# Performance work log

Hardware: AMD Instinct MI355X
Metric: run time of the kernel (lower is better)

Reference implementation:

```python
import jax, jax.numpy as jnp
import numpy as np

B, S, IN, EMB, H = 4, 2048, 256, 512, 8
D = EMB // H
SCALE = 1.0 / np.sqrt(EMB)  # source uses 1/sqrt(embed_size), not head_dim
EPS = 1e-5


def setup_inputs() -> dict:
    key = jax.random.key(0)
    ks = jax.random.split(key, 20)
    def w(k, shape, fan_in):
        return jax.random.normal(k, shape, jnp.float32) * (1.0 / np.sqrt(fan_in))
    inp = {"state_emb": jax.random.normal(ks[0], (B, S, IN), jnp.float32)}
    i = 1
    for p in ("q", "k", "v"):
        inp[f"{p}_W1"] = w(ks[i], (IN, EMB), IN); i += 1
        inp[f"{p}_b1"] = jnp.zeros((EMB,), jnp.float32)
        inp[f"{p}_W2"] = w(ks[i], (EMB, EMB), EMB); i += 1
        inp[f"{p}_b2"] = jnp.zeros((EMB,), jnp.float32)
    inp["f_W1"] = w(ks[i], (EMB, 2 * EMB), EMB); i += 1
    inp["f_b1"] = jnp.zeros((2 * EMB,), jnp.float32)
    inp["f_W2"] = w(ks[i], (2 * EMB, EMB), 2 * EMB); i += 1
    inp["f_b2"] = jnp.zeros((EMB,), jnp.float32)
    inp["ln1_g"] = jnp.ones((EMB,), jnp.float32)
    inp["ln1_b"] = jnp.zeros((EMB,), jnp.float32)
    inp["ln2_g"] = jnp.ones((EMB,), jnp.float32)
    inp["ln2_b"] = jnp.zeros((EMB,), jnp.float32)
    return inp


def _mlp2(x, W1, b1, W2, b2):
    return jax.nn.relu(x @ W1 + b1) @ W2 + b2


def _layernorm(x, g, b):
    mu = jnp.mean(x, axis=-1, keepdims=True)
    var = jnp.mean(jnp.square(x - mu), axis=-1, keepdims=True)
    return (x - mu) * jax.lax.rsqrt(var + EPS) * g + b


def reference(state_emb, q_W1, q_b1, q_W2, q_b2, k_W1, k_b1, k_W2, k_b2,
              v_W1, v_b1, v_W2, v_b2, f_W1, f_b1, f_W2, f_b2,
              ln1_g, ln1_b, ln2_g, ln2_b):
    n, dim = state_emb.shape[0], state_emb.shape[1]
    q = _mlp2(state_emb, q_W1, q_b1, q_W2, q_b2)  # [n, dim, EMB]
    k = _mlp2(state_emb, k_W1, k_b1, k_W2, k_b2)
    v = _mlp2(state_emb, v_W1, v_b1, v_W2, v_b2)
    qh = q.reshape(n, dim, H, D)
    kh = k.reshape(n, dim, H, D)
    vh = v.reshape(n, dim, H, D)
    energy = jnp.einsum('nqhd,nkhd->nhqk', qh, kh)  # [n, H, dim, dim]
    attn = jax.nn.softmax(energy * SCALE, axis=-1)
    ctx = jnp.einsum('nhql,nlhd->nqhd', attn, vh).reshape(n, dim, EMB)
    x = _layernorm(ctx + q, ln1_g, ln1_b)  # residual with queries, per source
    ff = _mlp2(x, f_W1, f_b1, f_W2, f_b2)
    return _layernorm(x + ff, ln2_g, ln2_b)
```

## Files before the change

### kernel.cpp

```cpp
#include <hip/hip_runtime.h>
#include <hip/hip_bf16.h>
#include <math.h>

#define BB   4
#define SS   2048
#define INF_ 256
#define EMB  512
#define NH   8
#define HD   64
#define NT   8192

typedef unsigned short u16;
typedef unsigned int   u32;
typedef __attribute__((ext_vector_type(8))) short bf16x8;
typedef __attribute__((ext_vector_type(8))) unsigned short u16x8;
typedef __attribute__((ext_vector_type(4))) float f32x4;

constexpr float C2  = 0.06375871607f;
constexpr float TB  = 1.00390625f;
constexpr float EPS = 1e-5f;

__device__ __forceinline__ u16 f2bf(float v) {
    __hip_bfloat16 h = __float2bfloat16(v);
    return *(u16*)&h;
}
__device__ __forceinline__ float bf2f(u16 u) {
    __hip_bfloat16 h = *(__hip_bfloat16*)&u;
    return __bfloat162float(h);
}
__device__ __forceinline__ u16 ftrunc_bf(float v) {
    return (u16)(__float_as_uint(v * TB) >> 16);
}
__device__ __forceinline__ f32x4 mfma16(bf16x8 a, bf16x8 b, f32x4 c) {
    return __builtin_amdgcn_mfma_f32_16x16x32_bf16(a, b, c, 0, 0, 0);
}
__device__ __forceinline__ void async16(const void* g, void* l) {
    __builtin_amdgcn_global_load_lds(
        (const __attribute__((address_space(1))) void*)g,
        (__attribute__((address_space(3))) void*)l, 16, 0, 0);
}
__device__ __forceinline__ int derive_flag(const u16* x) {
    const int lane = threadIdx.x & 63;
    const unsigned e = (x[lane * 2] >> 7) & 0xFF;
    float pl = (e == 0 || (e >= 110 && e <= 140)) ? 1.0f : 0.0f;
    #pragma unroll
    for (int o = 1; o < 64; o <<= 1) pl += __shfl_xor(pl, o);
    return pl < 32.0f;
}

__global__ __launch_bounds__(256) void prep(
    const u16* __restrict__ xsrc,
    const void* w0, const void* w1, const void* w2, const void* w3,
    const void* w4, const void* w5, const void* w6, const void* w7,
    const void* p0, const void* p1, const void* p2, const void* p3,
    const void* p4, const void* p5, const void* p6, const void* p7,
    const void* p8, const void* p9, const void* p10, const void* p11,
    u16* __restrict__ xbf, u16* __restrict__ wt1, u16* __restrict__ wt2,
    u16* __restrict__ f1t, u16* __restrict__ f2t, float* __restrict__ small)
{
    const int isf = derive_flag(xsrc);
    const int z = blockIdx.z;
    const int tid = threadIdx.x;

    if (z < 8) {
        int K, M; const void* src; u16* dst;
        switch (z) {
            case 0: K=256;  M=512;  src=w0; dst=wt1;             break;
            case 1: K=256;  M=512;  src=w1; dst=wt1+512*256;     break;
            case 2: K=256;  M=512;  src=w2; dst=wt1+2*512*256;   break;
            case 3: K=512;  M=512;  src=w3; dst=wt2;             break;
            case 4: K=512;  M=512;  src=w4; dst=wt2+512*512;     break;
            case 5: K=512;  M=512;  src=w5; dst=wt2+2*512*512;   break;
            case 6: K=512;  M=1024; src=w6; dst=f1t;             break;
            default:K=1024; M=512;  src=w7; dst=f2t;             break;
        }
        const int m0 = blockIdx.x * 32, k0 = blockIdx.y * 32;
        if (m0 >= M || k0 >= K) return;
        __shared__ u16 t[32][33];
        const int tx = tid & 31, ty = tid >> 5;
        #pragma unroll
        for (int i = 0; i < 4; ++i) {
            const int kk = k0 + ty + i * 8;
            t[ty + i * 8][tx] = isf ? ftrunc_bf(((const float*)src)[(size_t)kk * M + m0 + tx])
                                    : ((const u16*)src)[(size_t)kk * M + m0 + tx];
        }
        __syncthreads();
        #pragma unroll
        for (int i = 0; i < 4; ++i) {
            const int mm = m0 + ty + i * 8;
            dst[(size_t)mm * K + k0 + tx] = t[tx][ty + i * 8];
        }
    } else if (z == 8) {
        const int bid = blockIdx.y * 32 + blockIdx.x;
        const int base = bid * 2048 + tid * 8;
        if (isf) {
            #pragma unroll
            for (int j = 0; j < 8; ++j)
                xbf[base + j] = ftrunc_bf(((const float*)xsrc)[base + j]);
        } else {
            *(u16x8*)&xbf[base] = *(const u16x8*)&xsrc[base];
        }
    } else {
        const int bid = blockIdx.y * 32 + blockIdx.x;
        if (bid >= 28) return;
        const int e = bid * 256 + tid;
        int id, i;
        if (e < 3072)      { id = e >> 9;               i = e & 511;          }
        else if (e < 4096) { id = 6;                    i = e - 3072;         }
        else               { id = 7 + ((e - 4096) >> 9); i = (e - 4096) & 511; }
        const void* src;
        switch (id) {
            case 0: src = p0; break;  case 1: src = p1; break;
            case 2: src = p2; break;  case 3: src = p3; break;
            case 4: src = p4; break;  case 5: src = p5; break;
            case 6: src = p6; break;  case 7: src = p7; break;
            case 8: src = p8; break;  case 9: src = p9; break;
            case 10: src = p10; break; default: src = p11; break;
        }
        small[e] = isf ? ((const float*)src)[i] : bf2f(((const u16*)src)[i]);
    }
}

template <bool RELU, bool AWHICH, bool VOUT, bool SCALEK>
__global__ __launch_bounds__(256) void gemm64(
    const u16* __restrict__ Aall, const u16* __restrict__ Wtall,
    const float* __restrict__ ball, u16* __restrict__ out,
    u16* __restrict__ vtb, int N, int K, int M)
{
    __shared__ __align__(16) u16 sA[64 * 64];
    __shared__ __align__(16) u16 sB[64 * 64];

    const int mtiles = M >> 6;
    const int which = blockIdx.y / mtiles;
    const int colb  = blockIdx.y % mtiles;
    const int row0 = blockIdx.x << 6, col0 = colb << 6;
    const u16* A  = Aall + (AWHICH ? (size_t)which * N * K : 0);
    const u16* Wt = Wtall + (size_t)which * M * K;
    const float* bias = ball + (size_t)which * M;

    const int tid = threadIdx.x;
    const int lane = tid & 63, w = tid >> 6;
    const int wrow = (w & 1) << 5, wcol = (w >> 1) << 5;
    const int c = lane & 15, quad = lane >> 4;

    const u16* ap[2]; const u16* bp[2];
    #pragma unroll
    for (int i = 0; i < 2; ++i) {
        const int raw = i * 256 + tid, r = raw >> 3, ch = (raw & 7) ^ (r & 7);
        ap[i] = A + (size_t)(row0 + r) * K + ch * 8;
        bp[i] = Wt + (size_t)(col0 + r) * K + ch * 8;
    }

    f32x4 acc[2][2] = {};

    for (int k0 = 0; k0 < K; k0 += 64) {
        __syncthreads();
        #pragma unroll
        for (int i = 0; i < 2; ++i) {
            async16(ap[i], (char*)sA + (i * 256 + tid) * 16);
            ap[i] += 64;
            async16(bp[i], (char*)sB + (i * 256 + tid) * 16);
            bp[i] += 64;
        }
        __syncthreads();

        #pragma unroll
        for (int kt = 0; kt < 2; ++kt) {
            bf16x8 af[2], bfr[2];
            #pragma unroll
            for (int rt = 0; rt < 2; ++rt) {
                const int r = wrow + rt * 16 + c;
                af[rt] = *(const bf16x8*)&sA[(r * 8 + ((kt * 4 + quad) ^ (r & 7))) * 8];
            }
            #pragma unroll
            for (int ct = 0; ct < 2; ++ct) {
                const int r = wcol + ct * 16 + c;
                bfr[ct] = *(const bf16x8*)&sB[(r * 8 + ((kt * 4 + quad) ^ (r & 7))) * 8];
            }
            #pragma unroll
            for (int rt = 0; rt < 2; ++rt)
                #pragma unroll
                for (int ct = 0; ct < 2; ++ct)
                    acc[rt][ct] = mfma16(af[rt], bfr[ct], acc[rt][ct]);
        }
    }

    if (VOUT && which == 2) {
        __syncthreads();
        #pragma unroll
        for (int rt = 0; rt < 2; ++rt) {
            const int rowb = wrow + rt * 16 + quad * 4;
            #pragma unroll
            for (int ct = 0; ct < 2; ++ct) {
                const int col = wcol + ct * 16 + c;
                const float bb = bias[col0 + col];
                ushort4 pk;
                pk.x = ftrunc_bf(acc[rt][ct][0] + bb);
                pk.y = ftrunc_bf(acc[rt][ct][1] + bb);
                pk.z = ftrunc_bf(acc[rt][ct][2] + bb);
                pk.w = ftrunc_bf(acc[rt][ct][3] + bb);
                *(ushort4*)&sA[col * 72 + rowb] = pk;
            }
        }
        __syncthreads();
        const int dl = tid >> 2, part = tid & 3;
        const int hg = (col0 + dl) >> 6, dd = (col0 + dl) & 63;
        const int bb = row0 >> 11, s0 = row0 & 2047;
        u16* dst = vtb + ((size_t)(bb * NH + hg) * HD + dd) * SS + s0 + part * 16;
        #pragma unroll
        for (int j = 0; j < 2; ++j)
            *(u16x8*)&dst[j * 8] = *(const u16x8*)&sA[dl * 72 + part * 16 + j * 8];
        return;
    }

    const float sc = (SCALEK && which == 1) ? C2 : 1.0f;
    const size_t outW = (size_t)which * N * M;
    #pragma unroll
    for (int rt = 0; rt < 2; ++rt) {
        #pragma unroll
        for (int i = 0; i < 4; ++i) {
            const int row = row0 + wrow + rt * 16 + quad * 4 + i;
            #pragma unroll
            for (int ct = 0; ct < 2; ++ct) {
                const int col = col0 + wcol + ct * 16 + c;
                float v = (acc[rt][ct][i] + bias[col]) * sc;
                if (RELU) v = fmaxf(v, 0.0f);
                out[outW + (size_t)row * M + col] = ftrunc_bf(v);
            }
        }
    }
}

__global__ __launch_bounds__(512) void attn_mfma(
    const u16* __restrict__ q, const u16* __restrict__ k,
    const u16* __restrict__ vt, u16* __restrict__ ctx)
{
    __shared__ __align__(16) u16 sK[2][64 * 64];
    __shared__ __align__(16) u16 sV[2][64 * 64];
    __shared__ __align__(16) u16 sP[16][16 * 64];

    const int tid = threadIdx.x;
    const int w = tid >> 6, lane = tid & 63;
    const int c = lane & 15, quad = lane >> 4;
    const int id = blockIdx.x;
    const int slot = id >> 3;
    const int bh = ((id & 7) << 2) | (slot >> 3);
    const int qt = slot & 7;
    const int b = bh >> 3, h = bh & 7;
    const int q0 = qt * 256;
    const size_t tokbase = (size_t)b * SS;
    const int hoff = h * HD;

    bf16x8 qf[2][2];
    #pragma unroll
    for (int f = 0; f < 2; ++f) {
        const int myq = q0 + w * 32 + f * 16 + c;
        #pragma unroll
        for (int kt = 0; kt < 2; ++kt)
            qf[f][kt] = *(const bf16x8*)&q[(tokbase + myq) * EMB + hoff + kt * 32 + quad * 8];
    }

    union { u32 u[4]; bf16x8 v; } ones;
    #pragma unroll
    for (int i = 0; i < 4; ++i) ones.u[i] = 0x3F803F80u;

    const u16* kp; const u16* vp;
    {
        const int rr = tid >> 3, ch = (tid & 7) ^ (rr & 7);
        kp = k + (tokbase + rr) * EMB + hoff + ch * 8;
        vp = vt + ((size_t)(b * NH + h) * HD + rr) * SS + ch * 8;
    }
    auto stage = [&](int buf) {
        async16(kp, (char*)&sK[buf][0] + tid * 16);
        kp += 64 * EMB;
        async16(vp, (char*)&sV[buf][0] + tid * 16);
        vp += 64;
    };
    stage(0);

    f32x4 accO[2][4] = {};
    f32x4 accL[2] = {};
    const f32x4 zc = {};

    for (int t = 0; t < SS / 64; ++t) {
        __syncthreads();
        const int buf = t & 1;
        if (t + 1 < SS / 64) stage(buf ^ 1);

        f32x4 accS[2][4];
        #pragma unroll
        for (int mt = 0; mt < 4; ++mt) {
            const int key = mt * 16 + c;
            bf16x8 kf0 = *(const bf16x8*)&sK[buf][(key * 8 + (quad ^ (key & 7))) * 8];
            #pragma unroll
            for (int f = 0; f < 2; ++f)
                accS[f][mt] = mfma16(kf0, qf[f][0], zc);
            bf16x8 kf1 = *(const bf16x8*)&sK[buf][(key * 8 + ((4 + quad) ^ (key & 7))) * 8];
            #pragma unroll
            for (int f = 0; f < 2; ++f)
                accS[f][mt] = mfma16(kf1, qf[f][1], accS[f][mt]);
        }

        #pragma unroll
        for (int f = 0; f < 2; ++f) {
            u32 pw[8];
            #pragma unroll
            for (int mt = 0; mt < 4; ++mt) {
                const float e0 = __builtin_amdgcn_exp2f(accS[f][mt][0]);
                const float e1 = __builtin_amdgcn_exp2f(accS[f][mt][1]);
                const float e2 = __builtin_amdgcn_exp2f(accS[f][mt][2]);
                const float e3 = __builtin_amdgcn_exp2f(accS[f][mt][3]);
                pw[2 * mt]     = __builtin_amdgcn_perm(__float_as_uint(e1), __float_as_uint(e0), 0x07060302u);
                pw[2 * mt + 1] = __builtin_amdgcn_perm(__float_as_uint(e3), __float_as_uint(e2), 0x07060302u);
            }
            #pragma unroll
            for (int mt = 0; mt < 4; ++mt) {
                const int chunkW = 2 * mt + (quad >> 1);
                const int blk = c * 8 + (chunkW ^ (c & 7));
                uint2 u; u.x = pw[2 * mt]; u.y = pw[2 * mt + 1];
                *(uint2*)((char*)&sP[w * 2 + f][0] + blk * 16 + 8 * (quad & 1)) = u;
            }
        }

        bf16x8 pf[2][2];
        #pragma unroll
        for (int f = 0; f < 2; ++f) {
            #pragma unroll
            for (int kt = 0; kt < 2; ++kt)
                pf[f][kt] = *(const bf16x8*)&sP[w * 2 + f][(c * 8 + ((kt * 4 + quad) ^ (c & 7))) * 8];
            accL[f] = mfma16(ones.v, pf[f][0], accL[f]);
            accL[f] = mfma16(ones.v, pf[f][1], accL[f]);
        }
        #pragma unroll
        for (int nt = 0; nt < 4; ++nt) {
            const int d = nt * 16 + c;
            #pragma unroll
            for (int kt = 0; kt < 2; ++kt) {
                bf16x8 vf = *(const bf16x8*)&sV[buf][(d * 8 + ((kt * 4 + quad) ^ (d & 7))) * 8];
                #pragma unroll
                for (int f = 0; f < 2; ++f)
                    accO[f][nt] = mfma16(vf, pf[f][kt], accO[f][nt]);
            }
        }
    }

    #pragma unroll
    for (int f = 0; f < 2; ++f) {
        const float l = accL[f][0];
        const float li = (l > 0.0f) ? (1.0f / l) : 0.0f;
        const int tok = q0 + w * 32 + f * 16 + c;
        u16* dst = ctx + (tokbase + tok) * EMB + hoff + quad * 4;
        #pragma unroll
        for (int nt = 0; nt < 4; ++nt) {
            ushort4 pk;
            pk.x = ftrunc_bf(accO[f][nt][0] * li);
            pk.y = ftrunc_bf(accO[f][nt][1] * li);
            pk.z = ftrunc_bf(accO[f][nt][2] * li);
            pk.w = ftrunc_bf(accO[f][nt][3] * li);
            *(ushort4*)&dst[nt * 16] = pk;
        }
    }
}

__global__ __launch_bounds__(256) void ln_mid(
    const u16* __restrict__ a, const u16* __restrict__ b2,
    const float* __restrict__ g, const float* __restrict__ be,
    u16* __restrict__ outb)
{
    const int wave = threadIdx.x >> 6, lane = threadIdx.x & 63;
    const size_t row = (size_t)blockIdx.x * 4 + wave;
    const u16x8 av = *(const u16x8*)&a[row * EMB + lane * 8];
    const u16x8 bv = *(const u16x8*)&b2[row * EMB + lane * 8];
    float vals[8], sum = 0.0f;
    #pragma unroll
    for (int i = 0; i < 8; ++i) { vals[i] = bf2f(av[i]) + bf2f(bv[i]); sum += vals[i]; }
    #pragma unroll
    for (int o = 1; o < 64; o <<= 1) sum += __shfl_xor(sum, o);
    const float mu = sum * (1.0f / 512.0f);
    float vs = 0.0f;
    #pragma unroll
    for (int i = 0; i < 8; ++i) { const float d = vals[i] - mu; vs += d * d; }
    #pragma unroll
    for (int o = 1; o < 64; o <<= 1) vs += __shfl_xor(vs, o);
    const float rstd = rsqrtf(vs * (1.0f / 512.0f) + EPS);
    u16x8 ov;
    #pragma unroll
    for (int i = 0; i < 8; ++i) {
        const int col = lane * 8 + i;
        ov[i] = f2bf((vals[i] - mu) * rstd * g[col] + be[col]);
    }
    *(u16x8*)&outb[row * EMB + lane * 8] = ov;
}

__global__ __launch_bounds__(256) void ln_final(
    const u16* __restrict__ a, const u16* __restrict__ b2,
    const float* __restrict__ g, const float* __restrict__ be,
    void* __restrict__ dout, const u16* __restrict__ xsrc)
{
    const int isf = derive_flag(xsrc);
    const int wave = threadIdx.x >> 6, lane = threadIdx.x & 63;
    const size_t row = (size_t)blockIdx.x * 4 + wave;
    const u16x8 av = *(const u16x8*)&a[row * EMB + lane * 8];
    const u16x8 bv = *(const u16x8*)&b2[row * EMB + lane * 8];
    float vals[8], sum = 0.0f;
    #pragma unroll
    for (int i = 0; i < 8; ++i) { vals[i] = bf2f(av[i]) + bf2f(bv[i]); sum += vals[i]; }
    #pragma unroll
    for (int o = 1; o < 64; o <<= 1) sum += __shfl_xor(sum, o);
    const float mu = sum * (1.0f / 512.0f);
    float vs = 0.0f;
    #pragma unroll
    for (int i = 0; i < 8; ++i) { const float d = vals[i] - mu; vs += d * d; }
    #pragma unroll
    for (int o = 1; o < 64; o <<= 1) vs += __shfl_xor(vs, o);
    const float rstd = rsqrtf(vs * (1.0f / 512.0f) + EPS);
    if (isf) {
        #pragma unroll
        for (int i = 0; i < 8; ++i) {
            const int col = lane * 8 + i;
            ((float*)dout)[row * EMB + col] = (vals[i] - mu) * rstd * g[col] + be[col];
        }
    } else {
        u16x8 ov;
        #pragma unroll
        for (int i = 0; i < 8; ++i) {
            const int col = lane * 8 + i;
            ov[i] = f2bf((vals[i] - mu) * rstd * g[col] + be[col]);
        }
        *(u16x8*)&((u16*)dout)[row * EMB + lane * 8] = ov;
    }
}

extern "C" void kernel_launch(void* const* d_in, const int* in_sizes, int n_in,
                              void* d_out, int out_size, void* d_ws, size_t ws_size,
                              hipStream_t stream)
{
    char* ws = (char*)d_ws;
    float* small = (float*)(ws + 0);
    u16*   wt1   = (u16*)(ws + 32768);
    u16*   wt2   = (u16*)(ws + 819200);
    u16*   f1t   = (u16*)(ws + 2392064);
    u16*   f2t   = (u16*)(ws + 3440640);
    u16*   xbf   = (u16*)(ws + 4489216);
    u16*   h3    = (u16*)(ws + 8683520);
    u16*   qkv   = (u16*)(ws + 33849344);
    u16*   vtb   = (u16*)(ws + 59015168);
    u16*   ctxb  = (u16*)(ws + 67403776);
    u16*   x1b   = (u16*)(ws + 75792384);
    u16*   ffb   = (u16*)(ws + 84180992);

    const dim3 blk(256);
    const u16* xsrc = (const u16*)d_in[0];

    prep<<<dim3(32, 32, 10), blk, 0, stream>>>(
        xsrc,
        d_in[1], d_in[5], d_in[9], d_in[3], d_in[7], d_in[11], d_in[13], d_in[15],
        d_in[2], d_in[6], d_in[10], d_in[4], d_in[8], d_in[12],
        d_in[14], d_in[16], d_in[17], d_in[18], d_in[19], d_in[20],
        xbf, wt1, wt2, f1t, f2t, small);

    gemm64<true, false, false, false><<<dim3(128, 24), blk, 0, stream>>>(
        xbf, wt1, small + 0, h3, nullptr, NT, INF_, EMB);
    gemm64<false, true, true, true><<<dim3(128, 24), blk, 0, stream>>>(
        h3, wt2, small + 1536, qkv, vtb, NT, EMB, EMB);

    attn_mfma<<<dim3(256), dim3(512), 0, stream>>>(
        qkv, qkv + (size_t)NT * EMB, vtb, ctxb);

    ln_mid<<<NT / 4, blk, 0, stream>>>(ctxb, qkv, small + 4608, small + 5120, x1b);

    u16* h2 = h3;
    gemm64<true, false, false, false><<<dim3(128, 16), blk, 0, stream>>>(
        x1b, f1t, small + 3072, h2, nullptr, NT, EMB, 1024);
    gemm64<false, false, false, false><<<dim3(128, 8), blk, 0, stream>>>(
        h2, f2t, small + 4096, ffb, nullptr, NT, 1024, EMB);

    ln_final<<<NT / 4, blk, 0, stream>>>(x1b, ffb, small + 5632, small + 6144, d_out, xsrc);
}
```

Measured before the change: 245.8 us.

## Split attention key range across two wave groups with LDS reduction

The attention kernel now launches 1024 threads per block. Two groups of 8 waves each process half of the key sequence for the same 256 queries, and each group has its own K/V double buffers. At the end, group 1 writes its partial output and row sums to shared memory, and group 0 adds them and normalizes. This split-K scheme doubles the waves per block to hide latency better on only 256 blocks. In exchange it costs more LDS, a final cross-group reduction, and the larger block may limit occupancy.

```diff
diff --git a/kernel.cpp b/kernel.cpp
--- a/kernel.cpp
+++ b/kernel.cpp
@@ -231,16 +231,17 @@
     }
 }
 
-__global__ __launch_bounds__(512) void attn_mfma(
+__global__ __launch_bounds__(1024) void attn_mfma(
     const u16* __restrict__ q, const u16* __restrict__ k,
     const u16* __restrict__ vt, u16* __restrict__ ctx)
 {
-    __shared__ __align__(16) u16 sK[2][64 * 64];
-    __shared__ __align__(16) u16 sV[2][64 * 64];
-    __shared__ __align__(16) u16 sP[16][16 * 64];
+    __shared__ __align__(16) u16 sK[2][2][4096];
+    __shared__ __align__(16) u16 sV[2][2][4096];
+    __shared__ __align__(16) u16 sP[32][1024];
 
     const int tid = threadIdx.x;
-    const int w = tid >> 6, lane = tid & 63;
+    const int w16 = tid >> 6, lane = tid & 63;
+    const int g = w16 >> 3, w = w16 & 7;
     const int c = lane & 15, quad = lane >> 4;
     const int id = blockIdx.x;
     const int slot = id >> 3;
@@ -264,16 +265,17 @@
     #pragma unroll
     for (int i = 0; i < 4; ++i) ones.u[i] = 0x3F803F80u;
 
+    const int tig = tid & 511;
     const u16* kp; const u16* vp;
     {
-        const int rr = tid >> 3, ch = (tid & 7) ^ (rr & 7);
-        kp = k + (tokbase + rr) * EMB + hoff + ch * 8;
-        vp = vt + ((size_t)(b * NH + h) * HD + rr) * SS + ch * 8;
+        const int rr = tig >> 3, ch = (tig & 7) ^ (rr & 7);
+        kp = k + (tokbase + g * 1024 + rr) * EMB + hoff + ch * 8;
+        vp = vt + ((size_t)(b * NH + h) * HD + rr) * SS + g * 1024 + ch * 8;
     }
     auto stage = [&](int buf) {
-        async16(kp, (char*)&sK[buf][0] + tid * 16);
+        async16(kp, (char*)&sK[g][buf][0] + tig * 16);
         kp += 64 * EMB;
-        async16(vp, (char*)&sV[buf][0] + tid * 16);
+        async16(vp, (char*)&sV[g][buf][0] + tig * 16);
         vp += 64;
     };
     stage(0);
@@ -282,20 +284,20 @@
     f32x4 accL[2] = {};
     const f32x4 zc = {};
 
-    for (int t = 0; t < SS / 64; ++t) {
+    for (int t = 0; t < 16; ++t) {
         __syncthreads();
         const int buf = t & 1;
-        if (t + 1 < SS / 64) stage(buf ^ 1);
+        if (t + 1 < 16) stage(buf ^ 1);
 
         f32x4 accS[2][4];
         #pragma unroll
         for (int mt = 0; mt < 4; ++mt) {
             const int key = mt * 16 + c;
-            bf16x8 kf0 = *(const bf16x8*)&sK[buf][(key * 8 + (quad ^ (key & 7))) * 8];
+            bf16x8 kf0 = *(const bf16x8*)&sK[g][buf][(key * 8 + (quad ^ (key & 7))) * 8];
             #pragma unroll
             for (int f = 0; f < 2; ++f)
                 accS[f][mt] = mfma16(kf0, qf[f][0], zc);
-            bf16x8 kf1 = *(const bf16x8*)&sK[buf][(key * 8 + ((4 + quad) ^ (key & 7))) * 8];
+            bf16x8 kf1 = *(const bf16x8*)&sK[g][buf][(key * 8 + ((4 + quad) ^ (key & 7))) * 8];
             #pragma unroll
             for (int f = 0; f < 2; ++f)
                 accS[f][mt] = mfma16(kf1, qf[f][1], accS[f][mt]);
@@ -318,7 +320,7 @@
                 const int chunkW = 2 * mt + (quad >> 1);
                 const int blk = c * 8 + (chunkW ^ (c & 7));
                 uint2 u; u.x = pw[2 * mt]; u.y = pw[2 * mt + 1];
-                *(uint2*)((char*)&sP[w * 2 + f][0] + blk * 16 + 8 * (quad & 1)) = u;
+                *(uint2*)((char*)&sP[w16 * 2 + f][0] + blk * 16 + 8 * (quad & 1)) = u;
             }
         }
 
@@ -327,7 +329,7 @@
         for (int f = 0; f < 2; ++f) {
             #pragma unroll
             for (int kt = 0; kt < 2; ++kt)
-                pf[f][kt] = *(const bf16x8*)&sP[w * 2 + f][(c * 8 + ((kt * 4 + quad) ^ (c & 7))) * 8];
+                pf[f][kt] = *(const bf16x8*)&sP[w16 * 2 + f][(c * 8 + ((kt * 4 + quad) ^ (c & 7))) * 8];
             accL[f] = mfma16(ones.v, pf[f][0], accL[f]);
             accL[f] = mfma16(ones.v, pf[f][1], accL[f]);
         }
@@ -336,7 +338,7 @@
             const int d = nt * 16 + c;
             #pragma unroll
             for (int kt = 0; kt < 2; ++kt) {
-                bf16x8 vf = *(const bf16x8*)&sV[buf][(d * 8 + ((kt * 4 + quad) ^ (d & 7))) * 8];
+                bf16x8 vf = *(const bf16x8*)&sV[g][buf][(d * 8 + ((kt * 4 + quad) ^ (d & 7))) * 8];
                 #pragma unroll
                 for (int f = 0; f < 2; ++f)
                     accO[f][nt] = mfma16(vf, pf[f][kt], accO[f][nt]);
@@ -344,20 +346,41 @@
         }
     }
 
-    #pragma unroll
-    for (int f = 0; f < 2; ++f) {
-        const float l = accL[f][0];
-        const float li = (l > 0.0f) ? (1.0f / l) : 0.0f;
-        const int tok = q0 + w * 32 + f * 16 + c;
-        u16* dst = ctx + (tokbase + tok) * EMB + hoff + quad * 4;
-        #pragma unroll
-        for (int nt = 0; nt < 4; ++nt) {
-            ushort4 pk;
-            pk.x = ftrunc_bf(accO[f][nt][0] * li);
-            pk.y = ftrunc_bf(accO[f][nt][1] * li);
-            pk.z = ftrunc_bf(accO[f][nt][2] * li);
-            pk.w = ftrunc_bf(accO[f][nt][3] * li);
-            *(ushort4*)&dst[nt * 16] = pk;
+    __syncthreads();
+    float* mb = (float*)&sP[0][0];
+    float* ml = (float*)&sK[0][0][0];
+    if (g == 1) {
+        #pragma unroll
+        for (int f = 0; f < 2; ++f) {
+            const int mtok = w * 32 + f * 16 + c;
+            #pragma unroll
+            for (int nt = 0; nt < 4; ++nt) {
+                const int dcol = (nt * 16 + quad * 4) ^ ((mtok & 7) << 2);
+                *(f32x4*)&mb[mtok * 64 + dcol] = accO[f][nt];
+            }
+            if (quad == 0) ml[mtok] = accL[f][0];
+        }
+    }
+    __syncthreads();
+    if (g == 0) {
+        #pragma unroll
+        for (int f = 0; f < 2; ++f) {
+            const int mtok = w * 32 + f * 16 + c;
+            const float l = accL[f][0] + ml[mtok];
+            const float li = (l > 0.0f) ? (1.0f / l) : 0.0f;
+            const int tok = q0 + mtok;
+            u16* dst = ctx + (tokbase + tok) * EMB + hoff + quad * 4;
+            #pragma unroll
+            for (int nt = 0; nt < 4; ++nt) {
+                const int dcol = (nt * 16 + quad * 4) ^ ((mtok & 7) << 2);
+                const f32x4 pt = *(const f32x4*)&mb[mtok * 64 + dcol];
+                ushort4 pk;
+                pk.x = ftrunc_bf((accO[f][nt][0] + pt[0]) * li);
+                pk.y = ftrunc_bf((accO[f][nt][1] + pt[1]) * li);
+                pk.z = ftrunc_bf((accO[f][nt][2] + pt[2]) * li);
+                pk.w = ftrunc_bf((accO[f][nt][3] + pt[3]) * li);
+                *(ushort4*)&dst[nt * 16] = pk;
+            }
         }
     }
 }
@@ -464,7 +487,7 @@
     gemm64<false, true, true, true><<<dim3(128, 24), blk, 0, stream>>>(
         h3, wt2, small + 1536, qkv, vtb, NT, EMB, EMB);
 
-    attn_mfma<<<dim3(256), dim3(512), 0, stream>>>(
+    attn_mfma<<<dim3(256), dim3(1024), 0, stream>>>(
         qkv, qkv + (size_t)NT * EMB, vtb, ctxb);
 
     ln_mid<<<NT / 4, blk, 0, stream>>>(ctxb, qkv, small + 4608, small + 5120, x1b);
```

Result: faster. 227.6 us (-7.4%).
